# Kernel optimization log

Measured on AMD Instinct MI355X. Metric: run time of the kernel, lower is better.

The kernel has to match this reference:

```python
import jax, jax.numpy as jnp
import numpy as np

N, E, D, H, O = 100000, 1600000, 256, 128, 64


def setup_inputs() -> dict:
    key = jax.random.key(0)
    ks = jax.random.split(key, 10)
    x = jax.random.normal(ks[0], (N, D), dtype=jnp.float32)
    # edges without self loops (original adds remaining self loops itself)
    row = jax.random.randint(ks[1], (E,), 0, N)
    off = jax.random.randint(ks[2], (E,), 1, N)
    col = (row + off) % N
    edge_index = jnp.stack([row, col]).astype(jnp.int64)
    # positive PPMI edge weights (stand-in for cached random-walk PPMI values)
    ppmi_edge_weight = jax.random.uniform(ks[3], (E,), dtype=jnp.float32, minval=0.1, maxval=1.0)
    # glorot-style weights (shared between GCN and PPMI branches, as in the module)
    W1 = jax.random.normal(ks[4], (D, H), dtype=jnp.float32) * np.sqrt(2.0 / (D + H))
    b1 = jnp.zeros((H,), dtype=jnp.float32)
    W2 = jax.random.normal(ks[5], (H, O), dtype=jnp.float32) * np.sqrt(2.0 / (H + O))
    b2 = jnp.zeros((O,), dtype=jnp.float32)
    dense_w = jax.random.normal(ks[6], (O, 1), dtype=jnp.float32) * np.sqrt(2.0 / (O + 1))
    dense_b = jnp.zeros((1,), dtype=jnp.float32)
    return {"x": x, "edge_index": edge_index, "ppmi_edge_weight": ppmi_edge_weight,
            "W1": W1, "b1": b1, "W2": W2, "b2": b2,
            "dense_w": dense_w, "dense_b": dense_b}


def _sym_norm(row, col, ew, n):
    # deg^-0.5[row] * w * deg^-0.5[col], deg from scatter-add over source index
    deg = jax.ops.segment_sum(ew, row, num_segments=n)
    dis = jnp.where(deg > 0, deg ** -0.5, 0.0)
    return dis[row] * ew * dis[col]


def _gconv(h, W, b, row, col, norm, n):
    hw = h @ W                              # [N, F_out]
    msg = norm[:, None] * hw[row]           # gather + scale, [E', F_out]
    return jax.ops.segment_sum(msg, col, num_segments=n) + b


def reference(x, edge_index, ppmi_edge_weight, W1, b1, W2, b2, dense_w, dense_b):
    n = x.shape[0]
    row = edge_index[0].astype(jnp.int32)
    col = edge_index[1].astype(jnp.int32)
    sl = jnp.arange(n, dtype=jnp.int32)
    row_sl = jnp.concatenate([row, sl])
    col_sl = jnp.concatenate([col, sl])
    ones_sl = jnp.ones((n,), dtype=x.dtype)

    # GCN branch: edge_weight = 1, plus self loops (fill_value = 1)
    gcn_ew = jnp.concatenate([jnp.ones((row.shape[0],), dtype=x.dtype), ones_sl])
    gnorm = _sym_norm(row_sl, col_sl, gcn_ew, n)
    g = jax.nn.relu(_gconv(x, W1, b1, row_sl, col_sl, gnorm, n))  # dropout p in eval -> identity
    g = _gconv(g, W2, b2, row_sl, col_sl, gnorm, n)

    # PPMI branch: precomputed positive weights, plus self loops
    ppmi_ew = jnp.concatenate([ppmi_edge_weight.astype(x.dtype), ones_sl])
    pnorm = _sym_norm(row_sl, col_sl, ppmi_ew, n)
    p = jax.nn.relu(_gconv(x, W1, b1, row_sl, col_sl, pnorm, n))
    p = _gconv(p, W2, b2, row_sl, col_sl, pnorm, n)

    stacked = jnp.stack([g, p], axis=1)                 # [N, 2, O]
    logits = stacked @ dense_w + dense_b                # [N, 2, 1]
    w = jax.nn.softmax(logits, axis=1)
    return jnp.sum(stacked * w, axis=1)                 # [N, O]
```

## Files before the change

kernel.cpp:

```cpp
#include <hip/hip_runtime.h>
#include <hip/hip_bf16.h>
#include <math.h>

#define DD 256
#define HH 128
#define OO 64

#define EPB 8192
#define BKT 512
#define AWIN 512

typedef __attribute__((ext_vector_type(8))) __bf16 bf16x8;
typedef __attribute__((ext_vector_type(4))) __bf16 bf16x4;
typedef __attribute__((ext_vector_type(4))) float f32x4;
typedef __attribute__((ext_vector_type(2))) float f32x2;
typedef __attribute__((ext_vector_type(4))) int i32x4;

__device__ inline float2 bf2_to_f2(unsigned u) {
    float2 r;
    r.x = __uint_as_float(u << 16);
    r.y = __uint_as_float(u & 0xffff0000u);
    return r;
}

__global__ void part_count_kernel(const int* __restrict__ row, const int* __restrict__ col,
                                  int e, int nb,
                                  int* __restrict__ cnt_col, int* __restrict__ cnt_row) {
    __shared__ int hc[256], hr[256];
    int t = threadIdx.x;
    if (t < 256) { hc[t] = 0; hr[t] = 0; }
    __syncthreads();
    int base = blockIdx.x * EPB;
    int lim  = min(EPB, e - base);
    for (int i = t; i < lim; i += 512) {
        atomicAdd(&hc[col[base + i] >> 9], 1);
        atomicAdd(&hr[row[base + i] >> 9], 1);
    }
    __syncthreads();
    if (t < nb) {
        cnt_col[blockIdx.x * nb + t] = hc[t];
        cnt_row[blockIdx.x * nb + t] = hr[t];
    }
}

__global__ void scan_blocks_kernel(const int* __restrict__ cnt_col, const int* __restrict__ cnt_row,
                                   int* __restrict__ base_col, int* __restrict__ base_row,
                                   int* __restrict__ tot_col, int* __restrict__ tot_row,
                                   int nblk, int nb) {
    __shared__ int s[256];
    int side = (blockIdx.x >= (unsigned)nb) ? 1 : 0;
    int b = blockIdx.x - side * nb;
    const int* cnt = side ? cnt_row : cnt_col;
    int* base = side ? base_row : base_col;
    int* tot  = side ? tot_row  : tot_col;
    int t = threadIdx.x;
    int v = (t < nblk) ? cnt[(size_t)t * nb + b] : 0;
    s[t] = v;
    __syncthreads();
    for (int off = 1; off < 256; off <<= 1) {
        int u = (t >= off) ? s[t - off] : 0;
        __syncthreads();
        s[t] += u;
        __syncthreads();
    }
    if (t < nblk) base[(size_t)t * nb + b] = s[t] - v;
    if (t == 255) tot[b] = s[255];
}

__global__ void add_bases_kernel(int* __restrict__ base_col, int* __restrict__ base_row,
                                 const int* __restrict__ tot_col, const int* __restrict__ tot_row,
                                 int* __restrict__ bb_col, int* __restrict__ bb_row,
                                 int* __restrict__ row_ptr, int n, int e, int nblk, int nb) {
    __shared__ int s[256];
    __shared__ int bbv;
    int side = (blockIdx.x >= (unsigned)nb) ? 1 : 0;
    int b = blockIdx.x - side * nb;
    const int* tot = side ? tot_row : tot_col;
    int* base = side ? base_row : base_col;
    int t = threadIdx.x;
    int v = (t < nb) ? tot[t] : 0;
    s[t] = v;
    __syncthreads();
    for (int off = 1; off < 256; off <<= 1) {
        int u = (t >= off) ? s[t - off] : 0;
        __syncthreads();
        s[t] += u;
        __syncthreads();
    }
    if (t == 0) {
        bbv = (b > 0) ? s[b - 1] : 0;
        (side ? bb_row : bb_col)[b] = bbv;
    }
    __syncthreads();
    int add = bbv;
    for (int j = t; j < nblk; j += blockDim.x) base[(size_t)j * nb + b] += add;
    if (blockIdx.x == 0 && t == 0) row_ptr[n] = e;
}

__global__ void part_scatter_kernel(const int* __restrict__ row, const int* __restrict__ col,
                                    const float* __restrict__ ppmi,
                                    const int* __restrict__ base_col, const int* __restrict__ base_row,
                                    int4* __restrict__ tmp_col, int2* __restrict__ tmp_row,
                                    int e, int nb) {
    __shared__ int cc[256], cr[256];
    int t = threadIdx.x;
    if (t < nb) {
        cc[t] = base_col[blockIdx.x * nb + t];
        cr[t] = base_row[blockIdx.x * nb + t];
    }
    __syncthreads();
    int base = blockIdx.x * EPB;
    int lim  = min(EPB, e - base);
    for (int i = t; i < lim; i += 512) {
        int r = row[base + i], c = col[base + i];
        int w = __float_as_int(ppmi[base + i]);
        int sc = atomicAdd(&cc[c >> 9], 1);
        tmp_col[sc] = make_int4(c, r, w, 0);
        int sr = atomicAdd(&cr[r >> 9], 1);
        tmp_row[sr] = make_int2(r, w);
    }
}

__global__ void deg_bucket_kernel(const int2* __restrict__ tmp_row,
                                  const int* __restrict__ bb_row, const int* __restrict__ tot_row,
                                  float2* __restrict__ dis, int n) {
    __shared__ float dg[BKT], dp[BKT];
    int t = threadIdx.x;
    dg[t] = 1.0f; dp[t] = 1.0f;
    __syncthreads();
    int b = blockIdx.x;
    int beg = bb_row[b], cnt = tot_row[b];
    for (int i = t; i < cnt; i += 512) {
        int2 cell = tmp_row[beg + i];
        int lr = cell.x & (BKT - 1);
        atomicAdd(&dg[lr], 1.0f);
        atomicAdd(&dp[lr], __int_as_float(cell.y));
    }
    __syncthreads();
    int g = (b << 9) + t;
    if (g < n) dis[g] = make_float2(rsqrtf(dg[t]), rsqrtf(dp[t]));
}

__launch_bounds__(512)
__global__ void csr_bucket_kernel(const int4* __restrict__ tmp_col,
                                  const int* __restrict__ bb_col, const int* __restrict__ tot_col,
                                  const float2* __restrict__ dis,
                                  int* __restrict__ row_ptr, int4* __restrict__ csr_meta, int n) {
    __shared__ int hist[BKT], s[BKT], cur[BKT];
    int t = threadIdx.x;
    hist[t] = 0;
    __syncthreads();
    int b = blockIdx.x;
    int beg = bb_col[b], cnt = tot_col[b];
    for (int i = t; i < cnt; i += BKT) atomicAdd(&hist[tmp_col[beg + i].x & (BKT - 1)], 1);
    __syncthreads();
    int own = hist[t];
    s[t] = own;
    __syncthreads();
    for (int off = 1; off < BKT; off <<= 1) {
        int v = (t >= off) ? s[t - off] : 0;
        __syncthreads();
        s[t] += v;
        __syncthreads();
    }
    int gslot = beg + s[t] - own;
    cur[t] = gslot;
    int gc = (b << 9) + t;
    if (gc < n) row_ptr[gc] = gslot;
    __syncthreads();
    for (int i = t; i < cnt; i += BKT) {
        int4 cell = tmp_col[beg + i];
        int lc = cell.x & (BKT - 1);
        int slot = atomicAdd(&cur[lc], 1);
        int r = cell.y;
        float w = __int_as_float(cell.z);
        float2 d = dis[r];
        csr_meta[slot] = make_int4(r, __float_as_int(d.x), __float_as_int(d.y * w), 0);
    }
}

__global__ void conv_w_kernel(const float* __restrict__ W, __bf16* __restrict__ Bh,
                              __bf16* __restrict__ Bl, int K, int N) {
    int i = blockIdx.x * blockDim.x + threadIdx.x;
    if (i >= K * N) return;
    int k = i / N, nn = i % N;
    float v = W[i];
    __bf16 h = (__bf16)v;
    Bh[(size_t)nn * K + k] = h;
    Bl[(size_t)nn * K + k] = (__bf16)(v - (float)h);
}

template<int BN, int CS, typename OT, bool ILV>
__launch_bounds__(256, 4)
__global__ void mfma_gemm_reg_kernel(const float* __restrict__ A,
                                     const __bf16* __restrict__ Bth, const __bf16* __restrict__ Btl,
                                     OT* __restrict__ C, int M, int K, int nHalf) {
    constexpr int NT = BN / CS / 16;
    const int tid  = threadIdx.x;
    const int wave = tid >> 6;
    const int lane = tid & 63;
    const int quad = lane >> 4;
    const int l16  = lane & 15;
    const int gw   = blockIdx.x * 4 + wave;
    const int row0 = (gw / CS) * 32;
    const int cb   = (gw % CS) * (BN / CS);
    if (row0 >= M) return;

    f32x4 acc[2][NT] = {};

    const float* ap0 = A + (size_t)(row0 + l16) * K + quad * 8;
    const float* ap1 = A + (size_t)(row0 + 16 + l16) * K + quad * 8;

    float4 a0[2][2];
    a0[0][0] = *(const float4*)ap0;  a0[0][1] = *(const float4*)(ap0 + 4);
    a0[1][0] = *(const float4*)ap1;  a0[1][1] = *(const float4*)(ap1 + 4);

    for (int k0 = 0; k0 < K; k0 += 32) {
        float4 a1[2][2];
        if (k0 + 32 < K) {
            a1[0][0] = *(const float4*)(ap0 + k0 + 32);
            a1[0][1] = *(const float4*)(ap0 + k0 + 36);
            a1[1][0] = *(const float4*)(ap1 + k0 + 32);
            a1[1][1] = *(const float4*)(ap1 + k0 + 36);
        }
        bf16x8 bh[NT], bl[NT];
#pragma unroll
        for (int j = 0; j < NT; ++j) {
            size_t boff = (size_t)(cb + j * 16 + l16) * K + k0 + quad * 8;
            bh[j] = *(const bf16x8*)(Bth + boff);
            bl[j] = *(const bf16x8*)(Btl + boff);
        }
#pragma unroll
        for (int i = 0; i < 2; ++i) {
            float vv0 = a0[i][0].x, vv1 = a0[i][0].y, vv2 = a0[i][0].z, vv3 = a0[i][0].w;
            float vv4 = a0[i][1].x, vv5 = a0[i][1].y, vv6 = a0[i][1].z, vv7 = a0[i][1].w;
            __bf16 h0 = (__bf16)vv0, h1 = (__bf16)vv1, h2 = (__bf16)vv2, h3 = (__bf16)vv3;
            __bf16 h4 = (__bf16)vv4, h5 = (__bf16)vv5, h6 = (__bf16)vv6, h7 = (__bf16)vv7;
            bf16x8 ah = (bf16x8){h0, h1, h2, h3, h4, h5, h6, h7};
            bf16x8 al = (bf16x8){(__bf16)(vv0 - (float)h0), (__bf16)(vv1 - (float)h1),
                                 (__bf16)(vv2 - (float)h2), (__bf16)(vv3 - (float)h3),
                                 (__bf16)(vv4 - (float)h4), (__bf16)(vv5 - (float)h5),
                                 (__bf16)(vv6 - (float)h6), (__bf16)(vv7 - (float)h7)};
#pragma unroll
            for (int j = 0; j < NT; ++j) {
                acc[i][j] = __builtin_amdgcn_mfma_f32_16x16x32_bf16(ah, bh[j], acc[i][j], 0, 0, 0);
                acc[i][j] = __builtin_amdgcn_mfma_f32_16x16x32_bf16(ah, bl[j], acc[i][j], 0, 0, 0);
                acc[i][j] = __builtin_amdgcn_mfma_f32_16x16x32_bf16(al, bh[j], acc[i][j], 0, 0, 0);
            }
        }
        if (k0 + 32 < K) {
            a0[0][0] = a1[0][0]; a0[0][1] = a1[0][1];
            a0[1][0] = a1[1][0]; a0[1][1] = a1[1][1];
        }
    }

#pragma unroll
    for (int i = 0; i < 2; ++i) {
#pragma unroll
        for (int rg = 0; rg < 4; ++rg) {
            int gr = row0 + i * 16 + quad * 4 + rg;
            if constexpr (ILV) {
                int s = (gr >= nHalf) ? 1 : 0;
                size_t base = (size_t)(gr - s * nHalf) * (BN * 2) + s;
#pragma unroll
                for (int j = 0; j < NT; ++j)
                    C[base + (size_t)(cb + j * 16 + l16) * 2] = (OT)acc[i][j][rg];
            } else {
#pragma unroll
                for (int j = 0; j < NT; ++j)
                    C[(size_t)gr * BN + cb + j * 16 + l16] = (OT)acc[i][j][rg];
            }
        }
    }
}

__global__ void agg1_pull_kernel(const int* __restrict__ row_ptr, const int4* __restrict__ meta,
                                 const __bf16* __restrict__ hw1,
                                 const float2* __restrict__ dis,
                                 const float* __restrict__ b1,
                                 float* __restrict__ g_out, float* __restrict__ p_out, int n) {
    __shared__ i32x4 sm[AWIN];
    const int tid  = threadIdx.x;
    const int wave = tid >> 6;
    const int lane = tid & 63;
    const int c0   = blockIdx.x * 4;
    const int c    = c0 + wave;
    const int beg0 = row_ptr[c0];
    const int end3 = row_ptr[min(c0 + 4, n)];
    int beg = 0, end = 0;
    if (c < n) { beg = row_ptr[c]; end = row_ptr[c + 1]; }
    const int f2 = lane * 2;
    float sgx = 0.f, sgy = 0.f, spx = 0.f, spy = 0.f;

    for (int w = beg0; w < end3; w += AWIN) {
        const int cnt = min(AWIN, end3 - w);
        __syncthreads();
        for (int i = tid; i < cnt; i += 256)
            sm[i] = __builtin_nontemporal_load((const i32x4*)meta + w + i);
        __syncthreads();
        int t = max(beg, w);
        const int hi = min(end, w + cnt);
        for (; t + 8 <= hi; t += 8) {
            i32x4 m[8];
#pragma unroll
            for (int q = 0; q < 8; ++q) m[q] = sm[t - w + q];
            unsigned u[8];
#pragma unroll
            for (int q = 0; q < 8; ++q)
                u[q] = *(const unsigned*)(hw1 + ((size_t)(unsigned)m[q].x << 7) + f2);
#pragma unroll
            for (int q = 0; q < 8; ++q) {
                float2 h = bf2_to_f2(u[q]);
                float wg = __uint_as_float((unsigned)m[q].y);
                float wp = __uint_as_float((unsigned)m[q].z);
                sgx += wg * h.x; sgy += wg * h.y;
                spx += wp * h.x; spy += wp * h.y;
            }
        }
        if (t + 4 <= hi) {
            i32x4 m[4];
#pragma unroll
            for (int q = 0; q < 4; ++q) m[q] = sm[t - w + q];
            unsigned u[4];
#pragma unroll
            for (int q = 0; q < 4; ++q)
                u[q] = *(const unsigned*)(hw1 + ((size_t)(unsigned)m[q].x << 7) + f2);
#pragma unroll
            for (int q = 0; q < 4; ++q) {
                float2 h = bf2_to_f2(u[q]);
                float wg = __uint_as_float((unsigned)m[q].y);
                float wp = __uint_as_float((unsigned)m[q].z);
                sgx += wg * h.x; sgy += wg * h.y;
                spx += wp * h.x; spy += wp * h.y;
            }
            t += 4;
        }
        for (; t < hi; ++t) {
            i32x4 m0 = sm[t - w];
            float2 h0 = bf2_to_f2(*(const unsigned*)(hw1 + ((size_t)(unsigned)m0.x << 7) + f2));
            float wg0 = __uint_as_float((unsigned)m0.y);
            float wp0 = __uint_as_float((unsigned)m0.z);
            sgx += wg0 * h0.x; sgy += wg0 * h0.y;
            spx += wp0 * h0.x; spy += wp0 * h0.y;
        }
    }

    if (c < n) {
        float2 d = dis[c];
        size_t idx = ((size_t)c << 7) + f2;
        float2 hs = bf2_to_f2(*(const unsigned*)(hw1 + idx));
        float2 bv = *(const float2*)(b1 + f2);
        float gx = d.x * sgx + d.x * d.x * hs.x + bv.x;
        float gy = d.x * sgy + d.x * d.x * hs.y + bv.y;
        float px = d.y * spx + d.y * d.y * hs.x + bv.x;
        float py = d.y * spy + d.y * d.y * hs.y + bv.y;
        f32x2 go, po;
        go[0] = gx > 0.f ? gx : 0.f;  go[1] = gy > 0.f ? gy : 0.f;
        po[0] = px > 0.f ? px : 0.f;  po[1] = py > 0.f ? py : 0.f;
        __builtin_nontemporal_store(go, (f32x2*)(g_out + idx));
        __builtin_nontemporal_store(po, (f32x2*)(p_out + idx));
    }
}

__global__ void agg2_final_kernel(const int* __restrict__ row_ptr, const int4* __restrict__ meta,
                                  const __bf16* __restrict__ hw2i,
                                  const float2* __restrict__ dis,
                                  const float* __restrict__ b2,
                                  const float* __restrict__ dense_w, const float* __restrict__ dense_b,
                                  float* __restrict__ out, int n) {
    __shared__ i32x4 sm[AWIN];
    const int tid  = threadIdx.x;
    const int wave = tid >> 6;
    const int f    = tid & 63;
    const int c0   = blockIdx.x * 4;
    const int c    = c0 + wave;
    const int beg0 = row_ptr[c0];
    const int end3 = row_ptr[min(c0 + 4, n)];
    int beg = 0, end = 0;
    if (c < n) { beg = row_ptr[c]; end = row_ptr[c + 1]; }
    const int f2 = f * 2;
    float sg = 0.f, sp = 0.f;

    for (int w = beg0; w < end3; w += AWIN) {
        const int cnt = min(AWIN, end3 - w);
        __syncthreads();
        for (int i = tid; i < cnt; i += 256)
            sm[i] = __builtin_nontemporal_load((const i32x4*)meta + w + i);
        __syncthreads();
        int t = max(beg, w);
        const int hi = min(end, w + cnt);
        for (; t + 8 <= hi; t += 8) {
            i32x4 m[8];
#pragma unroll
            for (int q = 0; q < 8; ++q) m[q] = sm[t - w + q];
            unsigned u[8];
#pragma unroll
            for (int q = 0; q < 8; ++q)
                u[q] = *(const unsigned*)(hw2i + ((size_t)(unsigned)m[q].x << 7) + f2);
#pragma unroll
            for (int q = 0; q < 8; ++q) {
                float2 g0 = bf2_to_f2(u[q]);
                sg += __uint_as_float((unsigned)m[q].y) * g0.x;
                sp += __uint_as_float((unsigned)m[q].z) * g0.y;
            }
        }
        if (t + 4 <= hi) {
            i32x4 m[4];
#pragma unroll
            for (int q = 0; q < 4; ++q) m[q] = sm[t - w + q];
            unsigned u[4];
#pragma unroll
            for (int q = 0; q < 4; ++q)
                u[q] = *(const unsigned*)(hw2i + ((size_t)(unsigned)m[q].x << 7) + f2);
#pragma unroll
            for (int q = 0; q < 4; ++q) {
                float2 g0 = bf2_to_f2(u[q]);
                sg += __uint_as_float((unsigned)m[q].y) * g0.x;
                sp += __uint_as_float((unsigned)m[q].z) * g0.y;
            }
            t += 4;
        }
        for (; t < hi; ++t) {
            i32x4 m0 = sm[t - w];
            float2 g0 = bf2_to_f2(*(const unsigned*)(hw2i + ((size_t)(unsigned)m0.x << 7) + f2));
            sg += __uint_as_float((unsigned)m0.y) * g0.x;
            sp += __uint_as_float((unsigned)m0.z) * g0.y;
        }
    }

    if (c < n) {
        float2 d = dis[c];
        float2 gps = bf2_to_f2(*(const unsigned*)(hw2i + ((size_t)c << 7) + f2));
        float bb = b2[f];
        float gv = d.x * sg + d.x * d.x * gps.x + bb;
        float pv = d.y * sp + d.y * d.y * gps.y + bb;
        float dwv = dense_w[f];
        float lg = gv * dwv, lp = pv * dwv;
#pragma unroll
        for (int off = 32; off > 0; off >>= 1) {
            lg += __shfl_xor(lg, off, 64);
            lp += __shfl_xor(lp, off, 64);
        }
        lg += dense_b[0];
        lp += dense_b[0];
        float m  = fmaxf(lg, lp);
        float eg = expf(lg - m), ep = expf(lp - m);
        float wgt = eg / (eg + ep);
        __builtin_nontemporal_store(wgt * gv + (1.0f - wgt) * pv, out + (size_t)c * OO + f);
    }
}

extern "C" void kernel_launch(void* const* d_in, const int* in_sizes, int n_in,
                              void* d_out, int out_size, void* d_ws, size_t ws_size,
                              hipStream_t stream) {
    const float* x    = (const float*)d_in[0];
    const int*   ei   = (const int*)d_in[1];
    const float* ppmi = (const float*)d_in[2];
    const float* W1   = (const float*)d_in[3];
    const float* b1   = (const float*)d_in[4];
    const float* W2   = (const float*)d_in[5];
    const float* b2   = (const float*)d_in[6];
    const float* dw   = (const float*)d_in[7];
    const float* db   = (const float*)d_in[8];
    float* out = (float*)d_out;

    const int n = in_sizes[0] / DD;
    const int e = in_sizes[2];
    const int* row = ei;
    const int* col = ei + e;

    const int nb   = (n + BKT - 1) / BKT;
    const int nblk = (e + EPB - 1) / EPB;

    float* ws      = (float*)d_ws;
    float2* dis    = (float2*)ws;
    __bf16* hw1    = (__bf16*)(ws + 2 * (size_t)n);
    float* g1      = (float*)(hw1 + (size_t)n * HH);
    float* p1      = g1 + (size_t)n * HH;
    int4* csr_meta = (int4*)(p1 + (size_t)n * HH);
    __bf16* bt1h   = (__bf16*)(csr_meta + e);
    __bf16* bt1l   = bt1h + (size_t)DD * HH;
    __bf16* bt2h   = bt1l + (size_t)DD * HH;
    __bf16* bt2l   = bt2h + (size_t)HH * OO;
    int* row_ptr   = (int*)(bt2l + (size_t)HH * OO);
    int* cnt_col   = row_ptr + (n + 1);
    int* base_col  = cnt_col + (size_t)nblk * nb;
    int* cnt_row   = base_col + (size_t)nblk * nb;
    int* base_row  = cnt_row + (size_t)nblk * nb;
    int* bb_col    = base_row + (size_t)nblk * nb;
    int* tot_col   = bb_col + nb;
    int* bb_row    = tot_col + nb;
    int* tot_row   = bb_row + nb;
    int4* tmp_col  = (int4*)g1;
    int2* tmp_row  = (int2*)p1;
    __bf16* hw2i   = hw1;

    const int T = 256;

    part_count_kernel<<<nblk, 512, 0, stream>>>(row, col, e, nb, cnt_col, cnt_row);
    scan_blocks_kernel<<<2 * nb, T, 0, stream>>>(cnt_col, cnt_row, base_col, base_row,
                                                 tot_col, tot_row, nblk, nb);
    add_bases_kernel<<<2 * nb, T, 0, stream>>>(base_col, base_row, tot_col, tot_row,
                                               bb_col, bb_row, row_ptr, n, e, nblk, nb);
    part_scatter_kernel<<<nblk, 512, 0, stream>>>(row, col, ppmi, base_col, base_row,
                                                  tmp_col, tmp_row, e, nb);
    deg_bucket_kernel<<<nb, 512, 0, stream>>>(tmp_row, bb_row, tot_row, dis, n);
    csr_bucket_kernel<<<nb, BKT, 0, stream>>>(tmp_col, bb_col, tot_col, dis,
                                              row_ptr, csr_meta, n);

    conv_w_kernel<<<(DD * HH + T - 1) / T, T, 0, stream>>>(W1, bt1h, bt1l, DD, HH);
    conv_w_kernel<<<(HH * OO + T - 1) / T, T, 0, stream>>>(W2, bt2h, bt2l, HH, OO);

    {
        int waves1 = (n / 32) * 2;
        mfma_gemm_reg_kernel<HH, 2, __bf16, false><<<(waves1 + 3) / 4, 256, 0, stream>>>(
            x, bt1h, bt1l, hw1, n, DD, 0);
    }
    agg1_pull_kernel<<<(n + 3) / 4, 256, 0, stream>>>(row_ptr, csr_meta, hw1, dis, b1, g1, p1, n);
    {
        int waves2 = (2 * n) / 32;
        mfma_gemm_reg_kernel<OO, 1, __bf16, true><<<(waves2 + 3) / 4, 256, 0, stream>>>(
            g1, bt2h, bt2l, hw2i, 2 * n, HH, n);
    }
    agg2_final_kernel<<<(n + 3) / 4, 256, 0, stream>>>(row_ptr, csr_meta, hw2i, dis,
                                                       b2, dw, db, out, n);
}
```

Baseline: 547.1 us.

## Stage split-bf16 weight tiles in swizzled LDS for both MFMA GEMMs

Replaces the register-fed GEMM, in which every wave read its B (weight hi/lo) fragments directly from global memory, with a 512-thread block that first copies the block's column slice of both weight arrays into LDS using an XOR swizzle. All 8 waves then read B from LDS, and each wave still handles 32 rows. This is meant to cut redundant global and L2 traffic for the weights and to avoid LDS bank conflicts. In exchange each block uses up to 64 KB of LDS and pays a preload plus barrier, which can limit occupancy.

Result: faster. 501.2 us (-8.4%).

```diff
diff --git a/kernel.cpp b/kernel.cpp
--- a/kernel.cpp
+++ b/kernel.cpp
@@ -190,24 +190,41 @@
     Bl[(size_t)nn * K + k] = (__bf16)(v - (float)h);
 }
 
-template<int BN, int CS, typename OT, bool ILV>
-__launch_bounds__(256, 4)
-__global__ void mfma_gemm_reg_kernel(const float* __restrict__ A,
-                                     const __bf16* __restrict__ Bth, const __bf16* __restrict__ Btl,
-                                     OT* __restrict__ C, int M, int K, int nHalf) {
-    constexpr int NT = BN / CS / 16;
-    const int tid  = threadIdx.x;
+template<int BNp, int K, bool ILV>
+__launch_bounds__(512, 4)
+__global__ void mfma_gemm_ldsb_kernel(const float* __restrict__ A,
+                                      const __bf16* __restrict__ Bth, const __bf16* __restrict__ Btl,
+                                      __bf16* __restrict__ C, int M, int nHalf,
+                                      int ncg, int BNtot) {
+    constexpr int NT  = BNp / 16;
+    constexpr int GPC = K / 8;
+    __shared__ __bf16 Bs[2][BNp][K];
+
+    const int tid = threadIdx.x;
+    const int cg  = blockIdx.x % ncg;
+    const int rg  = blockIdx.x / ncg;
+    const int cb  = cg * BNp;
+
+    constexpr int TOT = 2 * BNp * GPC;
+    for (int i = tid; i < TOT; i += 512) {
+        int arr = i / (BNp * GPC);
+        int rem = i - arr * (BNp * GPC);
+        int c   = rem / GPC;
+        int g   = rem - c * GPC;
+        const __bf16* src = (arr ? Btl : Bth) + (size_t)(cb + c) * K + g * 8;
+        uint4 v = *(const uint4*)src;
+        *(uint4*)&Bs[arr][c][(g ^ (c & 7)) * 8] = v;
+    }
+    __syncthreads();
+
     const int wave = tid >> 6;
     const int lane = tid & 63;
     const int quad = lane >> 4;
     const int l16  = lane & 15;
-    const int gw   = blockIdx.x * 4 + wave;
-    const int row0 = (gw / CS) * 32;
-    const int cb   = (gw % CS) * (BN / CS);
+    const int row0 = rg * 256 + wave * 32;
     if (row0 >= M) return;
 
     f32x4 acc[2][NT] = {};
-
     const float* ap0 = A + (size_t)(row0 + l16) * K + quad * 8;
     const float* ap1 = A + (size_t)(row0 + 16 + l16) * K + quad * 8;
 
@@ -223,12 +240,14 @@
             a1[1][0] = *(const float4*)(ap1 + k0 + 32);
             a1[1][1] = *(const float4*)(ap1 + k0 + 36);
         }
+        const int g0 = (k0 >> 3) + quad;
         bf16x8 bh[NT], bl[NT];
 #pragma unroll
         for (int j = 0; j < NT; ++j) {
-            size_t boff = (size_t)(cb + j * 16 + l16) * K + k0 + quad * 8;
-            bh[j] = *(const bf16x8*)(Bth + boff);
-            bl[j] = *(const bf16x8*)(Btl + boff);
+            int c  = j * 16 + l16;
+            int gg = (g0 ^ (c & 7)) * 8;
+            bh[j] = *(const bf16x8*)&Bs[0][c][gg];
+            bl[j] = *(const bf16x8*)&Bs[1][c][gg];
         }
 #pragma unroll
         for (int i = 0; i < 2; ++i) {
@@ -257,18 +276,18 @@
 #pragma unroll
     for (int i = 0; i < 2; ++i) {
 #pragma unroll
-        for (int rg = 0; rg < 4; ++rg) {
-            int gr = row0 + i * 16 + quad * 4 + rg;
+        for (int rg2 = 0; rg2 < 4; ++rg2) {
+            int gr = row0 + i * 16 + quad * 4 + rg2;
             if constexpr (ILV) {
                 int s = (gr >= nHalf) ? 1 : 0;
-                size_t base = (size_t)(gr - s * nHalf) * (BN * 2) + s;
+                size_t base = (size_t)(gr - s * nHalf) * (BNtot * 2) + s;
 #pragma unroll
                 for (int j = 0; j < NT; ++j)
-                    C[base + (size_t)(cb + j * 16 + l16) * 2] = (OT)acc[i][j][rg];
+                    C[base + (size_t)(cb + j * 16 + l16) * 2] = (__bf16)acc[i][j][rg2];
             } else {
 #pragma unroll
                 for (int j = 0; j < NT; ++j)
-                    C[(size_t)gr * BN + cb + j * 16 + l16] = (OT)acc[i][j][rg];
+                    C[(size_t)gr * BNtot + cb + j * 16 + l16] = (__bf16)acc[i][j][rg2];
             }
         }
     }
@@ -512,15 +531,15 @@
     conv_w_kernel<<<(HH * OO + T - 1) / T, T, 0, stream>>>(W2, bt2h, bt2l, HH, OO);
 
     {
-        int waves1 = (n / 32) * 2;
-        mfma_gemm_reg_kernel<HH, 2, __bf16, false><<<(waves1 + 3) / 4, 256, 0, stream>>>(
-            x, bt1h, bt1l, hw1, n, DD, 0);
+        int nrg = (n + 255) / 256;
+        mfma_gemm_ldsb_kernel<64, 256, false><<<nrg * 2, 512, 0, stream>>>(
+            x, bt1h, bt1l, hw1, n, 0, 2, HH);
     }
     agg1_pull_kernel<<<(n + 3) / 4, 256, 0, stream>>>(row_ptr, csr_meta, hw1, dis, b1, g1, p1, n);
     {
-        int waves2 = (2 * n) / 32;
-        mfma_gemm_reg_kernel<OO, 1, __bf16, true><<<(waves2 + 3) / 4, 256, 0, stream>>>(
-            g1, bt2h, bt2l, hw2i, 2 * n, HH, n);
+        int nrg = (2 * n + 255) / 256;
+        mfma_gemm_ldsb_kernel<64, 128, true><<<nrg, 512, 0, stream>>>(
+            g1, bt2h, bt2l, hw2i, 2 * n, n, 1, OO);
     }
     agg2_final_kernel<<<(n + 3) / 4, 256, 0, stream>>>(row_ptr, csr_meta, hw2i, dis,
                                                        b2, dw, db, out, n);
```
